# Performance work log

Hardware: AMD Instinct MI355X
Metric: run time of the kernel (lower is better)

Reference implementation:

```python
import jax, jax.numpy as jnp
import numpy as np

D_IN_NUM = 16
D_IN_CAT = 16
D_OUT = 10
DIM = 512
N_FREQ = 32
FREQ_SCALE = 0.01
D_EMB = 48
TEMP = 1.0
CHUNK = 5000


def setup_inputs() -> dict:
    key = jax.random.key(0)
    ks = jax.random.split(key, 10)
    B, N = 1024, 40000
    d_in_total = D_IN_NUM * D_EMB + D_IN_CAT
    return {
        "x_num": jax.random.uniform(ks[0], (B, D_IN_NUM), dtype=jnp.float32),
        "x_cat": jax.random.uniform(ks[1], (B, D_IN_CAT), dtype=jnp.float32),
        "y": jax.random.randint(ks[2], (B,), 0, D_OUT),
        "candidate_x_num": jax.random.uniform(ks[3], (N, D_IN_NUM), dtype=jnp.float32),
        "candidate_x_cat": jax.random.uniform(ks[4], (N, D_IN_CAT), dtype=jnp.float32),
        "candidate_y": jax.random.randint(ks[5], (N,), 0, D_OUT),
        "frequencies": FREQ_SCALE * jax.random.normal(ks[6], (D_IN_NUM, N_FREQ), dtype=jnp.float32),
        "lin_w": 0.05 * jax.random.normal(ks[7], (2 * N_FREQ, D_EMB), dtype=jnp.float32),
        "lin_b": jnp.zeros((D_EMB,), dtype=jnp.float32),
        "enc_w": 0.02 * jax.random.normal(ks[8], (d_in_total, DIM), dtype=jnp.float32),
        "enc_b": jnp.zeros((DIM,), dtype=jnp.float32),
    }


def _plr_encode(x_num, x_cat, frequencies, lin_w, lin_b, enc_w, enc_b):
    # PLR 'lite' embedding: [B, F] -> [B, F, 2*n_freq] -> [B, F, d_emb]
    t = 2.0 * jnp.pi * frequencies[None] * x_num[:, :, None]        # [B,F,n_freq]
    feats = jnp.concatenate([jnp.cos(t), jnp.sin(t)], axis=-1)       # [B,F,2n_freq]
    emb = jax.nn.relu(feats @ lin_w + lin_b)                         # [B,F,d_emb]
    flat = emb.reshape(emb.shape[0], -1)                             # [B,F*d_emb]
    h = jnp.concatenate([flat, x_cat], axis=1) @ enc_w + enc_b       # [B,dim]
    return h


def reference(x_num, x_cat, y, candidate_x_num, candidate_x_cat, candidate_y,
              frequencies, lin_w, lin_b, enc_w, enc_b):
    q = _plr_encode(x_num, x_cat, frequencies, lin_w, lin_b, enc_w, enc_b)           # [B,dim]
    c = _plr_encode(candidate_x_num, candidate_x_cat, frequencies, lin_w, lin_b, enc_w, enc_b)  # [N,dim]
    cand_y = jax.nn.one_hot(candidate_y, D_OUT, dtype=jnp.float32)                   # [N,K]

    # pairwise Euclidean distance (matmul form, as torch.cdist)
    d2 = (jnp.sum(q * q, axis=1, keepdims=True)
          + jnp.sum(c * c, axis=1)[None, :]
          - 2.0 * q @ c.T)
    dist = jnp.sqrt(jnp.maximum(d2, 1e-12)) / TEMP                                   # [B,N]
    exp_d = jnp.exp(-dist)                                                           # [B,N]

    # original accumulates per-5000-chunk logsumexp of exp(-d) additively
    B, N = exp_d.shape
    n_chunks = N // CHUNK
    lse = jax.nn.logsumexp(exp_d.reshape(B, n_chunks, CHUNK), axis=-1).sum(axis=-1)  # [B]
    logits = exp_d @ cand_y                                                          # [B,K]
    return jnp.log(logits) - lse[:, None]
```

## Files before the change

### kernel.cpp

```cpp
#include <hip/hip_runtime.h>
#include <math.h>

typedef __attribute__((ext_vector_type(8))) short bf16x8;
typedef __attribute__((ext_vector_type(4))) float f32x4;
typedef unsigned short u16;
typedef unsigned int u32;

#define BQ 1024
#define NCAND 40000
#define ROWS_TOT 41024
#define NF 16
#define NFREQ 32
#define DEMB 48
#define KDIM 800
#define ASTRIDE 808
#define DIM 512
#define NCLS 10
#define NCHUNK 8
#define CHUNKSZ 5000
#define CT_PER_CHUNK 40
#define NCT 320
#define PSTRIDE 136
#define MROWS 64
#define TWO_PI 6.28318530717958647692f

__device__ __forceinline__ u16 f2bf(float f) {
  u32 u = __float_as_uint(f);
  u32 r = u + 0x7fffu + ((u >> 16) & 1u);
  return (u16)(r >> 16);
}
__device__ __forceinline__ float bf2f(u16 b) { return __uint_as_float(((u32)b) << 16); }
__device__ __forceinline__ u32 cvt_pk_bf16(float lo, float hi) {
  u32 r;
  asm("v_cvt_pk_bf16_f32 %0, %1, %2" : "=v"(r) : "v"(lo), "v"(hi));
  return r;
}

__global__ __launch_bounds__(256)
void k_prep(const float* __restrict__ enc_w, u16* __restrict__ enc_wT)
{
  __shared__ float tile[64][65];
  const int bk = blockIdx.x % 13;
  const int bn = blockIdx.x / 13;
#pragma unroll
  for (int e = 0; e < 16; ++e) {
    int r = e * 4 + (threadIdx.x >> 6);
    int c = threadIdx.x & 63;
    int k = bk * 64 + r;
    tile[r][c] = (k < 784) ? enc_w[k * DIM + bn * 64 + c] : 0.f;
  }
  __syncthreads();
#pragma unroll
  for (int e = 0; e < 16; ++e) {
    int r = e * 4 + (threadIdx.x >> 6);
    int c = threadIdx.x & 63;
    int k = bk * 64 + c;
    if (k < KDIM)
      enc_wT[(size_t)(bn * 64 + r) * KDIM + k] = f2bf(tile[c][r]);
  }
}

__global__ __launch_bounds__(512, 2)
void k_encode(const float* __restrict__ xq_num, const float* __restrict__ xq_cat,
              const float* __restrict__ xc_num, const float* __restrict__ xc_cat,
              const float* __restrict__ freq, const float* __restrict__ lin_w,
              const float* __restrict__ lin_b, const u16* __restrict__ enc_wT,
              const float* __restrict__ enc_b,
              u16* __restrict__ h_bf, float* __restrict__ norms)
{
  __shared__ u16 a_s[MROWS * ASTRIDE];
  __shared__ float norm_s[MROWS];

  const int t = threadIdx.x;
  const int row0 = blockIdx.x * MROWS;
  const bool isq = (row0 < BQ);
  const float* __restrict__ xnum = isq ? xq_num : xc_num;
  const float* __restrict__ xcat = isq ? xq_cat : xc_cat;
  const int rbase = isq ? row0 : (row0 - BQ);

  const int wid = t >> 6, l = t & 63, hi = l >> 4, lo = l & 15;

  if (t < MROWS) norm_s[t] = 0.f;
  for (int i = t; i < MROWS * 16; i += 512) {
    int r = i >> 4, c = i & 15;
    a_s[r * ASTRIDE + 768 + c] = f2bf(xcat[(rbase + r) * NF + c]);
  }
  for (int i = t; i < MROWS * 24; i += 512) {
    int r = i / 24, c = i - r * 24;
    a_s[r * ASTRIDE + 784 + c] = 0;
  }

  {
    float fq[8];
    *(float4*)&fq[0] = *(const float4*)&freq[lo * NFREQ + hi * 8];
    *(float4*)&fq[4] = *(const float4*)&freq[lo * NFREQ + hi * 8 + 4];
    float xv[8];
#pragma unroll
    for (int mi = 0; mi < 8; ++mi)
      xv[mi] = xnum[(rbase + wid * 8 + mi) * NF + lo];

    bf16x8 lwb[2][3];
#pragma unroll
    for (int kf = 0; kf < 2; ++kf)
#pragma unroll
      for (int nf = 0; nf < 3; ++nf)
#pragma unroll
        for (int e = 0; e < 8; ++e)
          lwb[kf][nf][e] = (short)f2bf(lin_w[(kf * 32 + hi * 8 + e) * DEMB + nf * 16 + lo]);
    float lb[3];
#pragma unroll
    for (int nf = 0; nf < 3; ++nf) lb[nf] = lin_b[nf * 16 + lo];

#pragma unroll
    for (int mi = 0; mi < 8; ++mi) {
      bf16x8 ac, as_;
#pragma unroll
      for (int e = 0; e < 8; ++e) {
        float tt = TWO_PI * fq[e] * xv[mi];
        ac[e] = (short)f2bf(__cosf(tt));
        as_[e] = (short)f2bf(__sinf(tt));
      }
#pragma unroll
      for (int nf = 0; nf < 3; ++nf) {
        f32x4 ec = {0.f, 0.f, 0.f, 0.f};
        ec = __builtin_amdgcn_mfma_f32_16x16x32_bf16(ac, lwb[0][nf], ec, 0, 0, 0);
        ec = __builtin_amdgcn_mfma_f32_16x16x32_bf16(as_, lwb[1][nf], ec, 0, 0, 0);
#pragma unroll
        for (int reg = 0; reg < 4; ++reg) {
          int f = hi * 4 + reg;
          int r = wid * 8 + mi;
          float v = fmaxf(ec[reg] + lb[nf], 0.f);
          a_s[r * ASTRIDE + f * DEMB + nf * 16 + lo] = f2bf(v);
        }
      }
    }
  }
  __syncthreads();

  f32x4 acc[4][4];
#pragma unroll
  for (int mf = 0; mf < 4; ++mf)
#pragma unroll
    for (int nf = 0; nf < 4; ++nf) acc[mf][nf] = 0.f;

  const u16* bwbase = enc_wT + (size_t)(wid * 64 + lo) * KDIM + hi * 8;
  const u16* asbase = a_s + lo * ASTRIDE + hi * 8;

  bf16x8 afb[3][4], bwb[3][4];

#define LOADK(kt, b)                                                          \
  {                                                                           \
    _Pragma("unroll")                                                         \
    for (int nf = 0; nf < 4; ++nf)                                            \
      bwb[b][nf] = *(const bf16x8*)(bwbase + (size_t)nf * 16 * KDIM + (kt) * 32); \
    _Pragma("unroll")                                                         \
    for (int mf = 0; mf < 4; ++mf)                                            \
      afb[b][mf] = *(const bf16x8*)(asbase + mf * 16 * ASTRIDE + (kt) * 32);  \
  }
#define MFMAK(b)                                                              \
  {                                                                           \
    _Pragma("unroll")                                                         \
    for (int mf = 0; mf < 4; ++mf)                                            \
      _Pragma("unroll")                                                       \
      for (int nf = 0; nf < 4; ++nf)                                          \
        acc[mf][nf] =                                                         \
            __builtin_amdgcn_mfma_f32_16x16x32_bf16(afb[b][mf], bwb[b][nf],   \
                                                    acc[mf][nf], 0, 0, 0);    \
  }

  LOADK(0, 0);
  LOADK(1, 1);
#pragma unroll
  for (int i = 0; i < 25; ++i) {
    if (i < 23) LOADK(i + 2, (i + 2) % 3);
    __builtin_amdgcn_s_setprio(1);
    MFMAK(i % 3);
    __builtin_amdgcn_s_setprio(0);
  }
#undef LOADK
#undef MFMAK

  float encb_v[4];
#pragma unroll
  for (int nf = 0; nf < 4; ++nf) encb_v[nf] = enc_b[wid * 64 + nf * 16 + lo];
  float nacc[4][4];
#pragma unroll
  for (int mf = 0; mf < 4; ++mf)
#pragma unroll
    for (int r = 0; r < 4; ++r) nacc[mf][r] = 0.f;

#pragma unroll
  for (int mf = 0; mf < 4; ++mf)
#pragma unroll
    for (int nf = 0; nf < 4; ++nf)
#pragma unroll
      for (int r = 0; r < 4; ++r) {
        int m = mf * 16 + hi * 4 + r;
        int n = wid * 64 + nf * 16 + lo;
        float hv = acc[mf][nf][r] + encb_v[nf];
        u16 ub = f2bf(hv);
        h_bf[(size_t)(row0 + m) * DIM + n] = ub;
        float hb = bf2f(ub);
        nacc[mf][r] = fmaf(hb, hb, nacc[mf][r]);
      }
#pragma unroll
  for (int mf = 0; mf < 4; ++mf)
#pragma unroll
    for (int r = 0; r < 4; ++r) {
      float v = nacc[mf][r];
      v += __shfl_xor(v, 1); v += __shfl_xor(v, 2);
      v += __shfl_xor(v, 4); v += __shfl_xor(v, 8);
      if (lo == 0) atomicAdd(&norm_s[mf * 16 + hi * 4 + r], v);
    }
  __syncthreads();
  if (t < MROWS) norms[row0 + t] = norm_s[t];
}

__global__ __launch_bounds__(256)
void k_dist(const u16* __restrict__ h_bf, const float* __restrict__ norms,
            const int* __restrict__ cand_y,
            float* __restrict__ cls_part, float* __restrict__ lse_part)
{
  __shared__ __align__(16) u16 AB_s[32768];
  __shared__ float qn_s[128];
  __shared__ float cn_s[128];
  __shared__ int cy_s[128];
  __shared__ float lse_s[128];

  u16* P_s = AB_s;

  const int flat = blockIdx.x;
  const int xcd = flat & 7;
  const int i = flat >> 3;
  const int ct = xcd * CT_PER_CHUNK + (i >> 3);
  const int qt = i & 7;

  const int t = threadIdx.x;
  const int chunk = xcd;
  const int ctl = ct - chunk * CT_PER_CHUNK;
  const int cand0 = chunk * CHUNKSZ + ctl * 128;
  const int cend = chunk * CHUNKSZ + CHUNKSZ;
  const int q0 = qt * 128;

  if (t < 128) {
    lse_s[t] = 0.f;
    qn_s[t] = norms[q0 + t];
    int j = cand0 + t; if (j > cend - 1) j = cend - 1;
    cn_s[t] = norms[BQ + j];
    cy_s[t] = cand_y[j];
  }

  const int wid = t >> 6, l = t & 63, hi = l >> 4, lo = l & 15;
  const int wc = wid & 1, wq = wid >> 1;

#define STAGE(dstoff, kt)                                                      \
  {                                                                            \
    _Pragma("unroll")                                                          \
    for (int p = 0; p < 4; ++p) {                                              \
      int seg = wid * 4 + p;                                                   \
      int lrow = seg * 8 + (l >> 3);                                           \
      int scol = ((l & 7) * 16) ^ ((lrow & 7) << 4);                           \
      int crow = cand0 + lrow; if (crow > cend - 1) crow = cend - 1;           \
      const u16* srcA = h_bf + (size_t)(BQ + crow) * DIM + (kt) * 64 + (scol >> 1); \
      __builtin_amdgcn_global_load_lds(                                        \
          (const __attribute__((address_space(1))) u32*)srcA,                  \
          (__attribute__((address_space(3))) u32*)(AB_s + (dstoff) + seg * 512), \
          16, 0, 0);                                                           \
      const u16* srcB = h_bf + (size_t)(q0 + lrow) * DIM + (kt) * 64 + (scol >> 1); \
      __builtin_amdgcn_global_load_lds(                                        \
          (const __attribute__((address_space(1))) u32*)srcB,                  \
          (__attribute__((address_space(3))) u32*)(AB_s + (dstoff) + 8192 + seg * 512), \
          16, 0, 0);                                                           \
    }                                                                          \
  }

  f32x4 acc[4][4];
#pragma unroll
  for (int mi = 0; mi < 4; ++mi)
#pragma unroll
    for (int ni = 0; ni < 4; ++ni) acc[mi][ni] = 0.f;

  STAGE(0, 0);
  STAGE(16384, 1);

#pragma unroll
  for (int kt = 0; kt < 8; ++kt) {
    if (kt == 7) asm volatile("s_waitcnt vmcnt(0)" ::: "memory");
    else         asm volatile("s_waitcnt vmcnt(8)" ::: "memory");
    __builtin_amdgcn_s_barrier();
    __builtin_amdgcn_sched_barrier(0);

    const u16* Ac = AB_s + (kt & 1) * 16384;
    const u16* Bc = Ac + 8192;
    __builtin_amdgcn_s_setprio(1);
#pragma unroll
    for (int ks = 0; ks < 2; ++ks) {
      bf16x8 af[4], bq[4];
#pragma unroll
      for (int mi = 0; mi < 4; ++mi) {
        int row = wc * 64 + mi * 16 + lo;
        int byt = (hi * 16 + ks * 64) ^ ((row & 7) << 4);
        af[mi] = *(const bf16x8*)&Ac[row * 64 + (byt >> 1)];
      }
#pragma unroll
      for (int ni = 0; ni < 4; ++ni) {
        int row = wq * 64 + ni * 16 + lo;
        int byt = (hi * 16 + ks * 64) ^ ((row & 7) << 4);
        bq[ni] = *(const bf16x8*)&Bc[row * 64 + (byt >> 1)];
      }
#pragma unroll
      for (int mi = 0; mi < 4; ++mi)
#pragma unroll
        for (int ni = 0; ni < 4; ++ni)
          acc[mi][ni] = __builtin_amdgcn_mfma_f32_16x16x32_bf16(af[mi], bq[ni], acc[mi][ni], 0, 0, 0);
    }
    __builtin_amdgcn_s_setprio(0);
    __builtin_amdgcn_sched_barrier(0);
    __builtin_amdgcn_s_barrier();
    if (kt < 6) STAGE((kt & 1) * 16384, kt + 2);
  }
#undef STAGE

  float qv[4];
#pragma unroll
  for (int ni = 0; ni < 4; ++ni) qv[ni] = qn_s[wq * 64 + ni * 16 + lo];

  u32 pk[4][4][2];
  float lacc[4] = {0.f, 0.f, 0.f, 0.f};
#pragma unroll
  for (int mi = 0; mi < 4; ++mi)
#pragma unroll
    for (int ni = 0; ni < 4; ++ni) {
      float ev[4];
#pragma unroll
      for (int r = 0; r < 4; ++r) {
        int crow = wc * 64 + mi * 16 + hi * 4 + r;
        bool valid = (cand0 + crow) < cend;
        float d2 = fmaf(-2.f, acc[mi][ni][r], cn_s[crow] + qv[ni]);
        float dist = __builtin_amdgcn_sqrtf(fmaxf(d2, 1e-12f));
        float e = valid ? __expf(-dist) : 0.f;
        ev[r] = e;
        lacc[ni] += valid ? __expf(e) : 0.f;
      }
      pk[mi][ni][0] = cvt_pk_bf16(ev[0], ev[1]);
      pk[mi][ni][1] = cvt_pk_bf16(ev[2], ev[3]);
    }

#pragma unroll
  for (int ni = 0; ni < 4; ++ni) {
    float v = lacc[ni];
    v += __shfl_xor(v, 16); v += __shfl_xor(v, 32);
    if (hi == 0) atomicAdd(&lse_s[wq * 64 + ni * 16 + lo], v);
  }

  __syncthreads();
#pragma unroll
  for (int mi = 0; mi < 4; ++mi)
#pragma unroll
    for (int ni = 0; ni < 4; ++ni) {
      int q = wq * 64 + ni * 16 + lo;
      int j0 = wc * 64 + mi * 16 + hi * 4;
      *(uint2*)&P_s[q * PSTRIDE + j0] = make_uint2(pk[mi][ni][0], pk[mi][ni][1]);
    }
  __syncthreads();

#pragma unroll
  for (int g = 0; g < 2; ++g) {
    f32x4 accc = {0.f, 0.f, 0.f, 0.f};
    const u16* Prow = P_s + (wid * 32 + g * 16 + lo) * PSTRIDE;
#pragma unroll
    for (int ks = 0; ks < 4; ++ks) {
      bf16x8 af = *(const bf16x8*)(Prow + ks * 32 + hi * 8);
      bf16x8 yb;
#pragma unroll
      for (int e = 0; e < 8; ++e) {
        int j = ks * 32 + hi * 8 + e;
        yb[e] = (short)((cy_s[j] == lo) ? 0x3F80 : 0);
      }
      accc = __builtin_amdgcn_mfma_f32_16x16x32_bf16(af, yb, accc, 0, 0, 0);
    }
    if (lo < NCLS) {
#pragma unroll
      for (int reg = 0; reg < 4; ++reg) {
        int qq = wid * 32 + g * 16 + hi * 4 + reg;
        cls_part[((size_t)ct * BQ + (q0 + qq)) * NCLS + lo] = accc[reg];
      }
    }
  }

  if (t < 128) lse_part[(size_t)ct * BQ + q0 + t] = lse_s[t];
}

__global__ __launch_bounds__(320)
void k_final(const float* __restrict__ cls_part, const float* __restrict__ lse_part,
             float* __restrict__ out)
{
  __shared__ float cls_sum[NCLS];
  __shared__ float ch_sum[NCHUNK];
  const int t = threadIdx.x;
  const int b = blockIdx.x;
  if (t < NCLS) cls_sum[t] = 0.f;
  if (t < NCHUNK) ch_sum[t] = 0.f;
  __syncthreads();

  float cs[NCLS];
#pragma unroll
  for (int c = 0; c < NCLS; ++c) cs[c] = cls_part[((size_t)t * BQ + b) * NCLS + c];
  float ls = lse_part[(size_t)t * BQ + b];
  atomicAdd(&ch_sum[t / CT_PER_CHUNK], ls);
#pragma unroll
  for (int c = 0; c < NCLS; ++c) {
    float w = cs[c];
    w += __shfl_xor(w, 1); w += __shfl_xor(w, 2); w += __shfl_xor(w, 4);
    w += __shfl_xor(w, 8); w += __shfl_xor(w, 16); w += __shfl_xor(w, 32);
    if ((t & 63) == 0) atomicAdd(&cls_sum[c], w);
  }
  __syncthreads();
  if (t < NCLS) {
    float lse = 0.f;
#pragma unroll
    for (int ch = 0; ch < NCHUNK; ++ch) lse += logf(ch_sum[ch]);
    out[b * NCLS + t] = logf(cls_sum[t]) - lse;
  }
}

extern "C" void kernel_launch(void* const* d_in, const int* in_sizes, int n_in,
                              void* d_out, int out_size, void* d_ws, size_t ws_size,
                              hipStream_t stream)
{
  const float* xq_num = (const float*)d_in[0];
  const float* xq_cat = (const float*)d_in[1];
  const float* xc_num = (const float*)d_in[3];
  const float* xc_cat = (const float*)d_in[4];
  const int* cand_y = (const int*)d_in[5];
  const float* freq = (const float*)d_in[6];
  const float* lin_w = (const float*)d_in[7];
  const float* lin_b = (const float*)d_in[8];
  const float* enc_w = (const float*)d_in[9];
  const float* enc_b = (const float*)d_in[10];

  u16* h_bf = (u16*)d_ws;
  float* norms = (float*)((char*)d_ws + (size_t)ROWS_TOT * DIM * 2);
  float* cls_part = norms + ROWS_TOT;
  float* lse_part = cls_part + (size_t)NCT * BQ * NCLS;
  u16* enc_wT = (u16*)(lse_part + (size_t)NCT * BQ);
  float* out = (float*)d_out;

  hipLaunchKernelGGL(k_prep, dim3(13 * 8), dim3(256), 0, stream, enc_w, enc_wT);
  hipLaunchKernelGGL(k_encode, dim3(ROWS_TOT / MROWS), dim3(512), 0, stream,
                     xq_num, xq_cat, xc_num, xc_cat, freq, lin_w, lin_b,
                     enc_wT, enc_b, h_bf, norms);
  hipLaunchKernelGGL(k_dist, dim3(NCT * 8), dim3(256), 0, stream,
                     h_bf, norms, cand_y, cls_part, lse_part);
  hipLaunchKernelGGL(k_final, dim3(BQ), dim3(320), 0, stream,
                     cls_part, lse_part, out);
}
```

Baseline: 182.8 us.

## Enlarge distance-kernel tile to 256x256 with 512 threads and fewer partials

The candidate-by-query distance kernel moves from 128x128 tiles with 256 threads to 256x256 tiles with 512 threads (8 waves). Each wave now holds 8x4 MFMA accumulators, and LDS staging buffers are doubled. The class-projection epilogue is split into two passes over the two candidate halves so P_s still fits in LDS. Halving the number of candidate tiles halves the partial outputs that k_final reduces. The aim is more operand reuse per global load and less partial-sum traffic. In exchange, register and LDS pressure rise: about 128KB of LDS per block likely allows only one block per CU, and the grid of 640 blocks may leave a tail imbalance.

Result: no change. 183.8 us (+0.5%).

```diff
diff --git a/kernel.cpp b/kernel.cpp
--- a/kernel.cpp
+++ b/kernel.cpp
@@ -18,8 +18,8 @@
 #define NCLS 10
 #define NCHUNK 8
 #define CHUNKSZ 5000
-#define CT_PER_CHUNK 40
-#define NCT 320
+#define CT2_PER_CHUNK 20
+#define NCT2 160
 #define PSTRIDE 136
 #define MROWS 64
 #define TWO_PI 6.28318530717958647692f
@@ -216,33 +216,33 @@
   if (t < MROWS) norms[row0 + t] = norm_s[t];
 }
 
-__global__ __launch_bounds__(256)
+__global__ __launch_bounds__(512, 2)
 void k_dist(const u16* __restrict__ h_bf, const float* __restrict__ norms,
             const int* __restrict__ cand_y,
             float* __restrict__ cls_part, float* __restrict__ lse_part)
 {
-  __shared__ __align__(16) u16 AB_s[32768];
-  __shared__ float qn_s[128];
-  __shared__ float cn_s[128];
-  __shared__ int cy_s[128];
-  __shared__ float lse_s[128];
+  __shared__ __align__(16) u16 AB_s[65536];
+  __shared__ float qn_s[256];
+  __shared__ float cn_s[256];
+  __shared__ int cy_s[256];
+  __shared__ float lse_s[256];
 
   u16* P_s = AB_s;
 
   const int flat = blockIdx.x;
   const int xcd = flat & 7;
   const int i = flat >> 3;
-  const int ct = xcd * CT_PER_CHUNK + (i >> 3);
-  const int qt = i & 7;
+  const int ctl = i >> 2;
+  const int qt = i & 3;
+  const int chunk = xcd;
+  const int ct2 = chunk * CT2_PER_CHUNK + ctl;
 
   const int t = threadIdx.x;
-  const int chunk = xcd;
-  const int ctl = ct - chunk * CT_PER_CHUNK;
-  const int cand0 = chunk * CHUNKSZ + ctl * 128;
+  const int cand0 = chunk * CHUNKSZ + ctl * 256;
   const int cend = chunk * CHUNKSZ + CHUNKSZ;
-  const int q0 = qt * 128;
-
-  if (t < 128) {
+  const int q0 = qt * 256;
+
+  if (t < 256) {
     lse_s[t] = 0.f;
     qn_s[t] = norms[q0 + t];
     int j = cand0 + t; if (j > cend - 1) j = cend - 1;
@@ -269,19 +269,19 @@
       const u16* srcB = h_bf + (size_t)(q0 + lrow) * DIM + (kt) * 64 + (scol >> 1); \
       __builtin_amdgcn_global_load_lds(                                        \
           (const __attribute__((address_space(1))) u32*)srcB,                  \
-          (__attribute__((address_space(3))) u32*)(AB_s + (dstoff) + 8192 + seg * 512), \
+          (__attribute__((address_space(3))) u32*)(AB_s + (dstoff) + 16384 + seg * 512), \
           16, 0, 0);                                                           \
     }                                                                          \
   }
 
-  f32x4 acc[4][4];
-#pragma unroll
-  for (int mi = 0; mi < 4; ++mi)
+  f32x4 acc[8][4];
+#pragma unroll
+  for (int mi = 0; mi < 8; ++mi)
 #pragma unroll
     for (int ni = 0; ni < 4; ++ni) acc[mi][ni] = 0.f;
 
   STAGE(0, 0);
-  STAGE(16384, 1);
+  STAGE(32768, 1);
 
 #pragma unroll
   for (int kt = 0; kt < 8; ++kt) {
@@ -290,15 +290,15 @@
     __builtin_amdgcn_s_barrier();
     __builtin_amdgcn_sched_barrier(0);
 
-    const u16* Ac = AB_s + (kt & 1) * 16384;
-    const u16* Bc = Ac + 8192;
+    const u16* Ac = AB_s + (kt & 1) * 32768;
+    const u16* Bc = Ac + 16384;
     __builtin_amdgcn_s_setprio(1);
 #pragma unroll
     for (int ks = 0; ks < 2; ++ks) {
-      bf16x8 af[4], bq[4];
-#pragma unroll
-      for (int mi = 0; mi < 4; ++mi) {
-        int row = wc * 64 + mi * 16 + lo;
+      bf16x8 af[8], bq[4];
+#pragma unroll
+      for (int mi = 0; mi < 8; ++mi) {
+        int row = wc * 128 + mi * 16 + lo;
         int byt = (hi * 16 + ks * 64) ^ ((row & 7) << 4);
         af[mi] = *(const bf16x8*)&Ac[row * 64 + (byt >> 1)];
       }
@@ -309,7 +309,7 @@
         bq[ni] = *(const bf16x8*)&Bc[row * 64 + (byt >> 1)];
       }
 #pragma unroll
-      for (int mi = 0; mi < 4; ++mi)
+      for (int mi = 0; mi < 8; ++mi)
 #pragma unroll
         for (int ni = 0; ni < 4; ++ni)
           acc[mi][ni] = __builtin_amdgcn_mfma_f32_16x16x32_bf16(af[mi], bq[ni], acc[mi][ni], 0, 0, 0);
@@ -317,7 +317,7 @@
     __builtin_amdgcn_s_setprio(0);
     __builtin_amdgcn_sched_barrier(0);
     __builtin_amdgcn_s_barrier();
-    if (kt < 6) STAGE((kt & 1) * 16384, kt + 2);
+    if (kt < 6) STAGE((kt & 1) * 32768, kt + 2);
   }
 #undef STAGE
 
@@ -325,16 +325,16 @@
 #pragma unroll
   for (int ni = 0; ni < 4; ++ni) qv[ni] = qn_s[wq * 64 + ni * 16 + lo];
 
-  u32 pk[4][4][2];
+  u32 pk[8][4][2];
   float lacc[4] = {0.f, 0.f, 0.f, 0.f};
 #pragma unroll
-  for (int mi = 0; mi < 4; ++mi)
+  for (int mi = 0; mi < 8; ++mi)
 #pragma unroll
     for (int ni = 0; ni < 4; ++ni) {
       float ev[4];
 #pragma unroll
       for (int r = 0; r < 4; ++r) {
-        int crow = wc * 64 + mi * 16 + hi * 4 + r;
+        int crow = wc * 128 + mi * 16 + hi * 4 + r;
         bool valid = (cand0 + crow) < cend;
         float d2 = fmaf(-2.f, acc[mi][ni][r], cn_s[crow] + qv[ni]);
         float dist = __builtin_amdgcn_sqrtf(fmaxf(d2, 1e-12f));
@@ -353,45 +353,51 @@
     if (hi == 0) atomicAdd(&lse_s[wq * 64 + ni * 16 + lo], v);
   }
 
-  __syncthreads();
-#pragma unroll
-  for (int mi = 0; mi < 4; ++mi)
-#pragma unroll
-    for (int ni = 0; ni < 4; ++ni) {
-      int q = wq * 64 + ni * 16 + lo;
-      int j0 = wc * 64 + mi * 16 + hi * 4;
-      *(uint2*)&P_s[q * PSTRIDE + j0] = make_uint2(pk[mi][ni][0], pk[mi][ni][1]);
-    }
-  __syncthreads();
-
-#pragma unroll
-  for (int g = 0; g < 2; ++g) {
-    f32x4 accc = {0.f, 0.f, 0.f, 0.f};
-    const u16* Prow = P_s + (wid * 32 + g * 16 + lo) * PSTRIDE;
-#pragma unroll
-    for (int ks = 0; ks < 4; ++ks) {
-      bf16x8 af = *(const bf16x8*)(Prow + ks * 32 + hi * 8);
-      bf16x8 yb;
-#pragma unroll
-      for (int e = 0; e < 8; ++e) {
-        int j = ks * 32 + hi * 8 + e;
-        yb[e] = (short)((cy_s[j] == lo) ? 0x3F80 : 0);
-      }
-      accc = __builtin_amdgcn_mfma_f32_16x16x32_bf16(af, yb, accc, 0, 0, 0);
-    }
-    if (lo < NCLS) {
+  f32x4 accc[2] = {{0.f, 0.f, 0.f, 0.f}, {0.f, 0.f, 0.f, 0.f}};
+#pragma unroll
+  for (int h = 0; h < 2; ++h) {
+    __syncthreads();
+    if (wc == h) {
+#pragma unroll
+      for (int mi = 0; mi < 8; ++mi)
+#pragma unroll
+        for (int ni = 0; ni < 4; ++ni) {
+          int q = wq * 64 + ni * 16 + lo;
+          int j0 = mi * 16 + hi * 4;
+          *(uint2*)&P_s[q * PSTRIDE + j0] = make_uint2(pk[mi][ni][0], pk[mi][ni][1]);
+        }
+    }
+    __syncthreads();
+#pragma unroll
+    for (int g = 0; g < 2; ++g) {
+      const u16* Prow = P_s + ((wid * 2 + g) * 16 + lo) * PSTRIDE;
+#pragma unroll
+      for (int ks = 0; ks < 4; ++ks) {
+        bf16x8 af = *(const bf16x8*)(Prow + ks * 32 + hi * 8);
+        bf16x8 yb;
+#pragma unroll
+        for (int e = 0; e < 8; ++e) {
+          int j = h * 128 + ks * 32 + hi * 8 + e;
+          yb[e] = (short)((cy_s[j] == lo) ? 0x3F80 : 0);
+        }
+        accc[g] = __builtin_amdgcn_mfma_f32_16x16x32_bf16(af, yb, accc[g], 0, 0, 0);
+      }
+    }
+  }
+  if (lo < NCLS) {
+#pragma unroll
+    for (int g = 0; g < 2; ++g)
 #pragma unroll
       for (int reg = 0; reg < 4; ++reg) {
-        int qq = wid * 32 + g * 16 + hi * 4 + reg;
-        cls_part[((size_t)ct * BQ + (q0 + qq)) * NCLS + lo] = accc[reg];
-      }
-    }
-  }
-
-  if (t < 128) lse_part[(size_t)ct * BQ + q0 + t] = lse_s[t];
-}
-
-__global__ __launch_bounds__(320)
+        int qq = (wid * 2 + g) * 16 + hi * 4 + reg;
+        cls_part[((size_t)ct2 * BQ + (q0 + qq)) * NCLS + lo] = accc[g][reg];
+      }
+  }
+
+  if (t < 256) lse_part[(size_t)ct2 * BQ + q0 + t] = lse_s[t];
+}
+
+__global__ __launch_bounds__(256)
 void k_final(const float* __restrict__ cls_part, const float* __restrict__ lse_part,
              float* __restrict__ out)
 {
@@ -404,10 +410,16 @@
   __syncthreads();
 
   float cs[NCLS];
-#pragma unroll
-  for (int c = 0; c < NCLS; ++c) cs[c] = cls_part[((size_t)t * BQ + b) * NCLS + c];
-  float ls = lse_part[(size_t)t * BQ + b];
-  atomicAdd(&ch_sum[t / CT_PER_CHUNK], ls);
+  float ls = 0.f;
+  if (t < NCT2) {
+#pragma unroll
+    for (int c = 0; c < NCLS; ++c) cs[c] = cls_part[((size_t)t * BQ + b) * NCLS + c];
+    ls = lse_part[(size_t)t * BQ + b];
+    atomicAdd(&ch_sum[t / CT2_PER_CHUNK], ls);
+  } else {
+#pragma unroll
+    for (int c = 0; c < NCLS; ++c) cs[c] = 0.f;
+  }
 #pragma unroll
   for (int c = 0; c < NCLS; ++c) {
     float w = cs[c];
@@ -442,16 +454,16 @@
   u16* h_bf = (u16*)d_ws;
   float* norms = (float*)((char*)d_ws + (size_t)ROWS_TOT * DIM * 2);
   float* cls_part = norms + ROWS_TOT;
-  float* lse_part = cls_part + (size_t)NCT * BQ * NCLS;
-  u16* enc_wT = (u16*)(lse_part + (size_t)NCT * BQ);
+  float* lse_part = cls_part + (size_t)NCT2 * BQ * NCLS;
+  u16* enc_wT = (u16*)(lse_part + (size_t)NCT2 * BQ);
   float* out = (float*)d_out;
 
   hipLaunchKernelGGL(k_prep, dim3(13 * 8), dim3(256), 0, stream, enc_w, enc_wT);
   hipLaunchKernelGGL(k_encode, dim3(ROWS_TOT / MROWS), dim3(512), 0, stream,
                      xq_num, xq_cat, xc_num, xc_cat, freq, lin_w, lin_b,
                      enc_wT, enc_b, h_bf, norms);
-  hipLaunchKernelGGL(k_dist, dim3(NCT * 8), dim3(256), 0, stream,
+  hipLaunchKernelGGL(k_dist, dim3(NCT2 * 4), dim3(512), 0, stream,
                      h_bf, norms, cand_y, cls_part, lse_part);
-  hipLaunchKernelGGL(k_final, dim3(BQ), dim3(320), 0, stream,
+  hipLaunchKernelGGL(k_final, dim3(BQ), dim3(256), 0, stream,
                      cls_part, lse_part, out);
 }
```
